# Kernel tuning notes

Hardware: AMD Instinct MI355X
Metric: run time of the kernel (lower is better)

The kernel has to match this reference:

```python
import jax, jax.numpy as jnp
import numpy as np

B, S, D, H = 8, 1024, 512, 12
HS = D // H  # 42 (head_size; 12*42 = 504 concat width, as in the original)


def setup_inputs() -> dict:
    key = jax.random.key(0)
    ks = jax.random.split(key, 12)
    sd = 0.02
    return {
        "embedded_patches": jax.random.normal(ks[0], (B, S, D), dtype=jnp.float32),
        # stacked per-head projections (12 independent Linear(D, HS, bias=False))
        "wk": jax.random.normal(ks[1], (H, D, HS), dtype=jnp.float32) * sd,
        "wq": jax.random.normal(ks[2], (H, D, HS), dtype=jnp.float32) * sd,
        "wv": jax.random.normal(ks[3], (H, D, HS), dtype=jnp.float32) * sd,
        "w_proj": jax.random.normal(ks[4], (H * HS, D), dtype=jnp.float32) * sd,  # [504, 512]
        "b_proj": jnp.zeros((D,), dtype=jnp.float32),
        # shared LayerNorm (same params used for both norms, as in the original)
        "gamma": jnp.ones((D,), dtype=jnp.float32),
        "beta": jnp.zeros((D,), dtype=jnp.float32),
        "w1": jax.random.normal(ks[5], (D, 4 * D), dtype=jnp.float32) * sd,
        "b1": jnp.zeros((4 * D,), dtype=jnp.float32),
        "w2": jax.random.normal(ks[6], (4 * D, D), dtype=jnp.float32) * sd,
        "b2": jnp.zeros((D,), dtype=jnp.float32),
    }


def _layernorm(x, gamma, beta, eps=1e-5):
    mu = jnp.mean(x, axis=-1, keepdims=True)
    var = jnp.var(x, axis=-1, keepdims=True)
    return (x - mu) * jax.lax.rsqrt(var + eps) * gamma + beta


def reference(embedded_patches, wk, wq, wv, w_proj, b_proj, gamma, beta, w1, b1, w2, b2):
    x = embedded_patches
    n1 = _layernorm(x, gamma, beta)
    # per-head projections, vectorized over heads: [B,S,D] x [H,D,E] -> [B,H,S,E]
    q = jnp.einsum('bsd,hde->bhse', n1, wq)
    k = jnp.einsum('bsd,hde->bhse', n1, wk)
    v = jnp.einsum('bsd,hde->bhse', n1, wv)
    scale = HS ** -0.5
    wei = jax.nn.softmax(jnp.einsum('bhse,bhte->bhst', q, k) * scale, axis=-1)
    out = jnp.einsum('bhst,bhte->bhse', wei, v)        # [B,H,S,E]
    out = out.transpose(0, 2, 1, 3).reshape(B, S, H * HS)  # concat heads -> [B,S,504]
    attn = out @ w_proj + b_proj                       # [B,S,D]
    # original quirk: takes batch element 0 and broadcasts against residual
    first_added = attn[0] + x                          # [S,D] + [B,S,D] -> [B,S,D]
    n2 = _layernorm(first_added, gamma, beta)
    h = jax.nn.gelu(n2 @ w1 + b1, approximate=False)   # torch nn.GELU default = exact erf
    ff = h @ w2 + b2
    return ff + first_added
```

## Files before the change

kernel.cpp:

```cpp
#include <hip/hip_runtime.h>
#include <hip/hip_bf16.h>
#include <stdint.h>


typedef unsigned short u16;
typedef __attribute__((ext_vector_type(8))) short short8;
typedef __attribute__((ext_vector_type(4))) float f32x4;

__device__ __forceinline__ u16 f2bf(float f) {
  union { float f; unsigned u; } x; x.f = f;
  return (u16)((x.u + 0x7FFFu + ((x.u >> 16) & 1u)) >> 16);
}
__device__ __forceinline__ float bf2f(u16 u) {
  union { unsigned u; float f; } x; x.u = ((unsigned)u) << 16;
  return x.f;
}

__device__ __forceinline__ void gload_lds16(const u16* g, u16* l) {
  __builtin_amdgcn_global_load_lds(
      (__attribute__((address_space(1))) void*)g,
      (__attribute__((address_space(3))) void*)l, 16, 0, 0);
}

__device__ __forceinline__ float wred_sum(float v) {
#pragma unroll
  for (int off = 32; off > 0; off >>= 1) v += __shfl_xor(v, off, 64);
  return v;
}
__device__ __forceinline__ float wred_max(float v) {
#pragma unroll
  for (int off = 32; off > 0; off >>= 1) v = fmaxf(v, __shfl_xor(v, off, 64));
  return v;
}

enum { EP_BF16 = 0, EP_PV = 1, EP_F32B = 2, EP_GELU = 3, EP_OUT = 4 };

template <int EP>
__launch_bounds__(256, 2)
__global__ void gemm_bt(const u16* __restrict__ A, int lda, long sAz,
                        const u16* __restrict__ Bt, int ldb, long sBz,
                        void* __restrict__ Cv, int ldc, long sCz,
                        int K, const float* __restrict__ bias,
                        const float* __restrict__ aux) {
  __shared__ u16 lA[128 * 32];
  __shared__ u16 lB[128 * 32];
  const int z = blockIdx.z;
  const u16* Ab = A + (long)z * sAz;
  const u16* Bb = Bt + (long)z * sBz;
  const int m0 = blockIdx.x * 128;
  const int n0 = blockIdx.y * 128;
  const int tid = threadIdx.x;
  const int w = tid >> 6;
  const int l = tid & 63;
  const int wr = w >> 1;
  const int wc = w & 1;

  f32x4 acc[4][4];
#pragma unroll
  for (int i = 0; i < 4; ++i)
#pragma unroll
    for (int j = 0; j < 4; ++j) acc[i][j] = (f32x4){0.f, 0.f, 0.f, 0.f};

  const int sm = w * 32 + (l >> 2);
  const int sk = (l & 3) * 8;
  const u16* ga0 = Ab + (long)(m0 + sm) * lda + sk;
  const u16* ga1 = Ab + (long)(m0 + sm + 16) * lda + sk;
  const u16* gb0 = Bb + (long)(n0 + sm) * ldb + sk;
  const u16* gb1 = Bb + (long)(n0 + sm + 16) * ldb + sk;
  u16* dA = &lA[w * 1024];
  u16* dB = &lB[w * 1024];

  const int aoff = (wr * 64 + (l & 15)) * 32 + (l >> 4) * 8;
  const int boff = (wc * 64 + (l & 15)) * 32 + (l >> 4) * 8;

  for (int k0 = 0; k0 < K; k0 += 32) {
    gload_lds16(ga0 + k0, dA);
    gload_lds16(ga1 + k0, dA + 512);
    gload_lds16(gb0 + k0, dB);
    gload_lds16(gb1 + k0, dB + 512);
    __syncthreads();
    short8 af[4], bfv[4];
#pragma unroll
    for (int mi = 0; mi < 4; ++mi)
      af[mi] = *(const short8*)&lA[aoff + mi * 16 * 32];
#pragma unroll
    for (int ni = 0; ni < 4; ++ni)
      bfv[ni] = *(const short8*)&lB[boff + ni * 16 * 32];
#pragma unroll
    for (int mi = 0; mi < 4; ++mi)
#pragma unroll
      for (int ni = 0; ni < 4; ++ni)
        acc[mi][ni] = __builtin_amdgcn_mfma_f32_16x16x32_bf16(
            af[mi], bfv[ni], acc[mi][ni], 0, 0, 0);
    __syncthreads();
  }

  const int rbase = m0 + wr * 64 + (l >> 4) * 4;
  const int cbase = n0 + wc * 64 + (l & 15);
#pragma unroll
  for (int mi = 0; mi < 4; ++mi) {
#pragma unroll
    for (int ni = 0; ni < 4; ++ni) {
#pragma unroll
      for (int j = 0; j < 4; ++j) {
        const int row = rbase + mi * 16 + j;
        const int col = cbase + ni * 16;
        const float v = acc[mi][ni][j];
        if (EP == EP_BF16) {
          ((u16*)Cv)[(long)z * sCz + (long)row * ldc + col] = f2bf(v);
        } else if (EP == EP_PV) {
          if (col < 42) {
            const float iv = aux[z * 1024 + row];
            ((u16*)Cv)[(long)row * ldc + z * 42 + col] = f2bf(v * iv);
          }
        } else if (EP == EP_F32B) {
          ((float*)Cv)[(long)row * ldc + col] = v + bias[col];
        } else if (EP == EP_GELU) {
          const float t = v + bias[col];
          const float g = 0.5f * t * (1.0f + erff(t * 0.70710678118654752f));
          ((u16*)Cv)[(long)row * ldc + col] = f2bf(g);
        } else {
          ((float*)Cv)[(long)row * ldc + col] =
              v + bias[col] + aux[(long)row * ldc + col];
        }
      }
    }
  }
}

__global__ void ln1_kernel(const float* __restrict__ x,
                           const float* __restrict__ gamma,
                           const float* __restrict__ beta,
                           u16* __restrict__ n1) {
  __shared__ float red[16];
  const int s = blockIdx.x;
  const int t = threadIdx.x;
  const float* row = x + (long)s * 512;
  const float v0 = row[t];
  const float v1 = row[t + 256];
  float sum = wred_sum(v0 + v1);
  float sq = wred_sum(v0 * v0 + v1 * v1);
  if ((t & 63) == 0) { red[t >> 6] = sum; red[8 + (t >> 6)] = sq; }
  __syncthreads();
  sum = red[0] + red[1] + red[2] + red[3];
  sq = red[8] + red[9] + red[10] + red[11];
  const float mu = sum * (1.0f / 512.0f);
  const float rstd = rsqrtf(sq * (1.0f / 512.0f) - mu * mu + 1e-5f);
  n1[(long)s * 512 + t] = f2bf((v0 - mu) * rstd * gamma[t] + beta[t]);
  n1[(long)s * 512 + t + 256] =
      f2bf((v1 - mu) * rstd * gamma[t + 256] + beta[t + 256]);
}

__global__ void ln2_kernel(const float* __restrict__ x,
                           const float* __restrict__ aproj,
                           const float* __restrict__ gamma,
                           const float* __restrict__ beta,
                           float* __restrict__ fa, u16* __restrict__ n2) {
  __shared__ float red[16];
  const int r = blockIdx.x;
  const int t = threadIdx.x;
  const int s = r & 1023;
  const float* xr = x + (long)r * 512;
  const float* ar = aproj + (long)s * 512;
  const float v0 = xr[t] + ar[t];
  const float v1 = xr[t + 256] + ar[t + 256];
  fa[(long)r * 512 + t] = v0;
  fa[(long)r * 512 + t + 256] = v1;
  float sum = wred_sum(v0 + v1);
  float sq = wred_sum(v0 * v0 + v1 * v1);
  if ((t & 63) == 0) { red[t >> 6] = sum; red[8 + (t >> 6)] = sq; }
  __syncthreads();
  sum = red[0] + red[1] + red[2] + red[3];
  sq = red[8] + red[9] + red[10] + red[11];
  const float mu = sum * (1.0f / 512.0f);
  const float rstd = rsqrtf(sq * (1.0f / 512.0f) - mu * mu + 1e-5f);
  n2[(long)r * 512 + t] = f2bf((v0 - mu) * rstd * gamma[t] + beta[t]);
  n2[(long)r * 512 + t + 256] =
      f2bf((v1 - mu) * rstd * gamma[t + 256] + beta[t + 256]);
}

__global__ void softmax_kernel(u16* __restrict__ SP, float* __restrict__ invl) {
  __shared__ float red[16];
  const long row = blockIdx.x;
  u16* p = SP + row * 1024;
  const int t = threadIdx.x;
  uint2 u = ((const uint2*)p)[t];
  const float s0 = bf2f((u16)(u.x & 0xffff));
  const float s1 = bf2f((u16)(u.x >> 16));
  const float s2 = bf2f((u16)(u.y & 0xffff));
  const float s3 = bf2f((u16)(u.y >> 16));
  float m = wred_max(fmaxf(fmaxf(s0, s1), fmaxf(s2, s3)));
  if ((t & 63) == 0) red[t >> 6] = m;
  __syncthreads();
  m = fmaxf(fmaxf(red[0], red[1]), fmaxf(red[2], red[3]));
  const float e0 = __expf(s0 - m), e1 = __expf(s1 - m);
  const float e2 = __expf(s2 - m), e3 = __expf(s3 - m);
  float sum = wred_sum(e0 + e1 + e2 + e3);
  if ((t & 63) == 0) red[8 + (t >> 6)] = sum;
  __syncthreads();
  sum = red[8] + red[9] + red[10] + red[11];
  if (t == 0) invl[row] = 1.0f / sum;
  uint2 o;
  o.x = (unsigned)f2bf(e0) | ((unsigned)f2bf(e1) << 16);
  o.y = (unsigned)f2bf(e2) | ((unsigned)f2bf(e3) << 16);
  ((uint2*)p)[t] = o;
}

__global__ void prep_qkv_kernel(const float* __restrict__ wq,
                                const float* __restrict__ wk,
                                u16* __restrict__ BtQKV, float scale) {
  const int i = blockIdx.x * 256 + threadIdx.x;
  const int n = i >> 9, d = i & 511;
  const int pq = n / 768;
  const int h = (n % 768) >> 6;
  const int e = n & 63;
  float v = 0.f;
  if (e < 42) {
    v = (pq ? wk : wq)[((long)h * 512 + d) * 42 + e];
    if (!pq) v *= scale;
  }
  BtQKV[i] = f2bf(v);
}
__global__ void prep_wvT_kernel(const float* __restrict__ wv,
                                u16* __restrict__ wvT) {
  const int i = blockIdx.x * 256 + threadIdx.x;
  const int r = i >> 9, d = i & 511;
  const int h = r >> 7, e = r & 127;
  wvT[i] = f2bf(e < 42 ? wv[((long)h * 512 + d) * 42 + e] : 0.f);
}
__global__ void prep_proj_kernel(const float* __restrict__ wp,
                                 u16* __restrict__ BtP) {
  const int i = blockIdx.x * 256 + threadIdx.x;
  const int n = i >> 9, k = i & 511;
  BtP[i] = f2bf(k < 504 ? wp[(long)k * 512 + n] : 0.f);
}
__global__ void prep_w1_kernel(const float* __restrict__ w1,
                               u16* __restrict__ Bt1) {
  const int i = blockIdx.x * 256 + threadIdx.x;
  const int n = i >> 9, k = i & 511;
  Bt1[i] = f2bf(w1[(long)k * 2048 + n]);
}
__global__ void prep_w2_kernel(const float* __restrict__ w2,
                               u16* __restrict__ Bt2) {
  const int i = blockIdx.x * 256 + threadIdx.x;
  const int n = i >> 11, k = i & 2047;
  Bt2[i] = f2bf(w2[(long)k * 512 + n]);
}
__global__ void zero_u16_kernel(u16* __restrict__ p) {
  p[blockIdx.x * 256 + threadIdx.x] = 0;
}

extern "C" void kernel_launch(void* const* d_in, const int* in_sizes, int n_in,
                              void* d_out, int out_size, void* d_ws,
                              size_t ws_size, hipStream_t stream) {
  const float* x = (const float*)d_in[0];
  const float* wk = (const float*)d_in[1];
  const float* wq = (const float*)d_in[2];
  const float* wv = (const float*)d_in[3];
  const float* w_proj = (const float*)d_in[4];
  const float* b_proj = (const float*)d_in[5];
  const float* gamma = (const float*)d_in[6];
  const float* beta = (const float*)d_in[7];
  const float* w1 = (const float*)d_in[8];
  const float* b1 = (const float*)d_in[9];
  const float* w2 = (const float*)d_in[10];
  const float* b2 = (const float*)d_in[11];

  char* base = (char*)d_ws;
  size_t off = 0;
  auto alloc = [&](size_t bytes) -> void* {
    void* p = base + off;
    off += (bytes + 255) & ~(size_t)255;
    return p;
  };
  u16* n1 = (u16*)alloc(1024L * 512 * 2);
  u16* qkvc = (u16*)alloc(1024L * 1536 * 2);
  u16* SP = (u16*)alloc(12L * 1024 * 1024 * 2);
  u16* wvT = (u16*)alloc(1536L * 512 * 2);
  u16* vt = (u16*)alloc(1536L * 1024 * 2);
  u16* cat = (u16*)alloc(1024L * 512 * 2);
  float* aproj = (float*)alloc(1024L * 512 * 4);
  float* fa = (float*)alloc(8192L * 512 * 4);
  u16* n2 = (u16*)alloc(8192L * 512 * 2);
  u16* hbuf = (u16*)alloc(8192L * 2048 * 2);
  u16* BtQKV = (u16*)alloc(1536L * 512 * 2);
  u16* BtP = (u16*)alloc(512L * 512 * 2);
  u16* Bt1 = (u16*)alloc(2048L * 512 * 2);
  u16* Bt2 = (u16*)alloc(512L * 2048 * 2);
  float* invl = (float*)alloc(12L * 1024 * 4);
  (void)ws_size; (void)in_sizes; (void)n_in; (void)out_size;

  const float scale = 0.15430334996209191f;

  prep_qkv_kernel<<<3072, 256, 0, stream>>>(wq, wk, BtQKV, scale);
  prep_wvT_kernel<<<3072, 256, 0, stream>>>(wv, wvT);
  prep_proj_kernel<<<1024, 256, 0, stream>>>(w_proj, BtP);
  prep_w1_kernel<<<4096, 256, 0, stream>>>(w1, Bt1);
  prep_w2_kernel<<<4096, 256, 0, stream>>>(w2, Bt2);
  zero_u16_kernel<<<2048, 256, 0, stream>>>(cat);
  ln1_kernel<<<1024, 256, 0, stream>>>(x, gamma, beta, n1);

  gemm_bt<EP_BF16><<<dim3(8, 12, 1), 256, 0, stream>>>(
      n1, 512, 0, BtQKV, 512, 0, qkvc, 1536, 0, 512, nullptr, nullptr);
  gemm_bt<EP_BF16><<<dim3(12, 8, 1), 256, 0, stream>>>(
      wvT, 512, 0, n1, 512, 0, vt, 1024, 0, 512, nullptr, nullptr);
  gemm_bt<EP_BF16><<<dim3(8, 8, 12), 256, 0, stream>>>(
      qkvc, 1536, 64, qkvc + 768, 1536, 64, SP, 1024, 1024L * 1024, 64,
      nullptr, nullptr);
  softmax_kernel<<<12288, 256, 0, stream>>>(SP, invl);
  gemm_bt<EP_PV><<<dim3(8, 1, 12), 256, 0, stream>>>(
      SP, 1024, 1024L * 1024, vt, 1024, 128L * 1024, cat, 512, 0, 1024,
      nullptr, invl);
  gemm_bt<EP_F32B><<<dim3(8, 4, 1), 256, 0, stream>>>(
      cat, 512, 0, BtP, 512, 0, aproj, 512, 0, 512, b_proj, nullptr);
  ln2_kernel<<<8192, 256, 0, stream>>>(x, aproj, gamma, beta, fa, n2);
  gemm_bt<EP_GELU><<<dim3(64, 16, 1), 256, 0, stream>>>(
      n2, 512, 0, Bt1, 512, 0, hbuf, 2048, 0, 512, b1, nullptr);
  gemm_bt<EP_OUT><<<dim3(64, 4, 1), 256, 0, stream>>>(
      hbuf, 2048, 0, Bt2, 2048, 0, d_out, 512, 0, 2048, b2, fa);
}
```

Baseline: 195.2 us.

## Use 256x256 double-buffered pipelined GEMM with split-K for FFN layers

Adds a new 512-thread GEMM kernel with 256x256 tiles, K-step 64, XOR-swizzled LDS, double buffering, direct global-to-LDS loads interleaved with MFMA phases, and priority hints. It replaces the two FFN GEMMs. The second GEMM is split in two along K into fp32 partials, which a separate combine kernel sums with the bias and residual. This aims to raise MFMA utilisation and data reuse on the dominant FFN work. The cost is extra partial-buffer traffic, one extra launch, and a write of part into the start of d_ws, which may overlap buffers carved out of the same workspace.

```diff
diff --git a/kernel.cpp b/kernel.cpp
--- a/kernel.cpp
+++ b/kernel.cpp
@@ -33,7 +33,175 @@
   return v;
 }
 
-enum { EP_BF16 = 0, EP_PV = 1, EP_F32B = 2, EP_GELU = 3, EP_OUT = 4 };
+#define MFMA16x16(a, b, c) __builtin_amdgcn_mfma_f32_16x16x32_bf16(a, b, c, 0, 0, 0)
+
+enum { G8_GELU = 0, G8_F32 = 1 };
+
+template <int EP>
+__device__ __forceinline__ void read_af8(short8 (&af)[8], const u16* half,
+                                         int aBase, int s0, int s1) {
+  const char* hc = (const char*)half;
+#pragma unroll
+  for (int mi = 0; mi < 4; ++mi) {
+    af[mi * 2 + 0] = *(const short8*)(hc + aBase + mi * 2048 + s0);
+    af[mi * 2 + 1] = *(const short8*)(hc + aBase + mi * 2048 + s1);
+  }
+}
+template <int EP>
+__device__ __forceinline__ void read_bf4(short8 (&bf)[4], const u16* half,
+                                         int bBase, int s0, int s1) {
+  const char* hc = (const char*)half;
+#pragma unroll
+  for (int ni = 0; ni < 2; ++ni) {
+    bf[ni * 2 + 0] = *(const short8*)(hc + bBase + ni * 2048 + s0);
+    bf[ni * 2 + 1] = *(const short8*)(hc + bBase + ni * 2048 + s1);
+  }
+}
+template <int MH, int NH>
+__device__ __forceinline__ void do_mfma16(f32x4 (&acc)[8][4],
+                                          const short8 (&af)[8],
+                                          const short8 (&bf)[4]) {
+#pragma unroll
+  for (int mi = 0; mi < 4; ++mi)
+#pragma unroll
+    for (int ni = 0; ni < 2; ++ni)
+#pragma unroll
+      for (int ks = 0; ks < 2; ++ks)
+        acc[MH * 4 + mi][NH * 2 + ni] =
+            MFMA16x16(af[mi * 2 + ks], bf[ni * 2 + ks], acc[MH * 4 + mi][NH * 2 + ni]);
+}
+
+__device__ __forceinline__ void stage_half(const u16* src, int ld, u16* halfdst,
+                                           int w, int l) {
+  const int r0 = w * 8 + (l >> 3);
+  const int ce = ((l & 7) ^ (l >> 3)) * 8;
+  gload_lds16(src + (long)r0 * ld + ce, halfdst + w * 512);
+  gload_lds16(src + (long)(r0 + 64) * ld + ce, halfdst + (8 + w) * 512);
+}
+
+#define H_A0 0
+#define H_B0 1
+#define H_B1 2
+#define H_A1 3
+
+template <int EP>
+__launch_bounds__(512, 2)
+__global__ void gemm8(const u16* __restrict__ A, int lda, long sAz,
+                      const u16* __restrict__ Bt, int ldb, long sBz,
+                      void* __restrict__ Cv, int ldc, long sCz, int K,
+                      const float* __restrict__ bias) {
+  __shared__ u16 lds[2 * 4 * 8192];
+  const int z = blockIdx.z;
+  const u16* Ab = A + (long)z * sAz;
+  const u16* Bb = Bt + (long)z * sBz;
+  const int m0 = blockIdx.x * 256;
+  const int n0 = blockIdx.y * 256;
+  const int tid = threadIdx.x;
+  const int w = tid >> 6;
+  const int l = tid & 63;
+  const int wm = w >> 2;
+  const int wn = w & 3;
+  const int NT = K >> 6;
+
+  const int aBase = (wm * 64 + (l & 15)) * 128;
+  const int bBase = (wn * 32 + (l & 15)) * 128;
+  const int s0 = (((l >> 4)) ^ (l & 7)) * 16;
+  const int s1 = ((4 + (l >> 4)) ^ (l & 7)) * 16;
+
+  f32x4 acc[8][4];
+#pragma unroll
+  for (int i = 0; i < 8; ++i)
+#pragma unroll
+    for (int j = 0; j < 4; ++j) acc[i][j] = (f32x4){0.f, 0.f, 0.f, 0.f};
+
+  short8 af[8], bf0[4], bf1[4];
+
+  stage_half(Ab + (long)m0 * lda, lda, lds + H_A0 * 8192, w, l);
+  stage_half(Bb + (long)n0 * ldb, ldb, lds + H_B0 * 8192, w, l);
+  stage_half(Bb + (long)(n0 + 128) * ldb, ldb, lds + H_B1 * 8192, w, l);
+  stage_half(Ab + (long)(m0 + 128) * lda, lda, lds + H_A1 * 8192, w, l);
+
+  for (int t = 0; t < NT; ++t) {
+    u16* cur = lds + (t & 1) * 32768;
+    u16* nxt = lds + ((t & 1) ^ 1) * 32768;
+    const int tn = (t + 1 == NT) ? 0 : (t + 1);
+    const u16* An = Ab + tn * 64;
+    const u16* Bn = Bb + tn * 64;
+
+    asm volatile("s_waitcnt vmcnt(4)" ::: "memory");
+    __builtin_amdgcn_s_barrier();
+    __builtin_amdgcn_sched_barrier(0);
+    read_af8<EP>(af, cur + H_A0 * 8192, aBase, s0, s1);
+    read_bf4<EP>(bf0, cur + H_B0 * 8192, bBase, s0, s1);
+    stage_half(An + (long)m0 * lda, lda, nxt + H_A0 * 8192, w, l);
+    asm volatile("s_waitcnt lgkmcnt(0)" ::: "memory");
+    __builtin_amdgcn_sched_barrier(0);
+    __builtin_amdgcn_s_setprio(1);
+    do_mfma16<0, 0>(acc, af, bf0);
+    __builtin_amdgcn_s_setprio(0);
+
+    asm volatile("s_waitcnt vmcnt(4)" ::: "memory");
+    __builtin_amdgcn_s_barrier();
+    __builtin_amdgcn_sched_barrier(0);
+    read_bf4<EP>(bf1, cur + H_B1 * 8192, bBase, s0, s1);
+    stage_half(Bn + (long)n0 * ldb, ldb, nxt + H_B0 * 8192, w, l);
+    asm volatile("s_waitcnt lgkmcnt(0)" ::: "memory");
+    __builtin_amdgcn_sched_barrier(0);
+    __builtin_amdgcn_s_setprio(1);
+    do_mfma16<0, 1>(acc, af, bf1);
+    __builtin_amdgcn_s_setprio(0);
+
+    asm volatile("s_waitcnt vmcnt(4)" ::: "memory");
+    __builtin_amdgcn_s_barrier();
+    __builtin_amdgcn_sched_barrier(0);
+    read_af8<EP>(af, cur + H_A1 * 8192, aBase, s0, s1);
+    stage_half(Bn + (long)(n0 + 128) * ldb, ldb, nxt + H_B1 * 8192, w, l);
+    stage_half(An + (long)(m0 + 128) * lda, lda, nxt + H_A1 * 8192, w, l);
+    asm volatile("s_waitcnt lgkmcnt(0)" ::: "memory");
+    __builtin_amdgcn_sched_barrier(0);
+    __builtin_amdgcn_s_setprio(1);
+    do_mfma16<1, 0>(acc, af, bf0);
+    do_mfma16<1, 1>(acc, af, bf1);
+    __builtin_amdgcn_s_setprio(0);
+  }
+  asm volatile("s_waitcnt vmcnt(0)" ::: "memory");
+
+  const int rb = m0 + wm * 64 + ((l >> 4) << 2);
+  const int cb = n0 + wn * 32 + (l & 15);
+#pragma unroll
+  for (int mi = 0; mi < 8; ++mi) {
+    const int row = rb + (mi >> 2) * 128 + (mi & 3) * 16;
+#pragma unroll
+    for (int ni = 0; ni < 4; ++ni) {
+      const int col = cb + (ni >> 1) * 128 + (ni & 1) * 16;
+#pragma unroll
+      for (int j = 0; j < 4; ++j) {
+        const float v = acc[mi][ni][j];
+        if (EP == G8_GELU) {
+          const float tt = v + bias[col];
+          const float g = 0.5f * tt * (1.0f + erff(tt * 0.70710678118654752f));
+          ((u16*)Cv)[(long)(row + j) * ldc + col] = f2bf(g);
+        } else {
+          ((float*)Cv)[(long)z * sCz + (long)(row + j) * ldc + col] = v;
+        }
+      }
+    }
+  }
+}
+
+__global__ void combine_kernel(const float* __restrict__ p,
+                               const float* __restrict__ fa,
+                               const float* __restrict__ b2,
+                               float* __restrict__ out) {
+  const long i = (long)blockIdx.x * 256 + threadIdx.x;
+  const f32x4 a = ((const f32x4*)p)[i];
+  const f32x4 b = ((const f32x4*)(p + 8192L * 512))[i];
+  const f32x4 f = ((const f32x4*)fa)[i];
+  const f32x4 bb = ((const f32x4*)b2)[i & 127];
+  ((f32x4*)out)[i] = a + b + f + bb;
+}
+
+enum { EP_BF16 = 0, EP_PV = 1, EP_F32B = 2 };
 
 template <int EP>
 __launch_bounds__(256, 2)
@@ -90,8 +258,7 @@
     for (int mi = 0; mi < 4; ++mi)
 #pragma unroll
       for (int ni = 0; ni < 4; ++ni)
-        acc[mi][ni] = __builtin_amdgcn_mfma_f32_16x16x32_bf16(
-            af[mi], bfv[ni], acc[mi][ni], 0, 0, 0);
+        acc[mi][ni] = MFMA16x16(af[mi], bfv[ni], acc[mi][ni]);
     __syncthreads();
   }
 
@@ -113,15 +280,8 @@
             const float iv = aux[z * 1024 + row];
             ((u16*)Cv)[(long)row * ldc + z * 42 + col] = f2bf(v * iv);
           }
-        } else if (EP == EP_F32B) {
+        } else {
           ((float*)Cv)[(long)row * ldc + col] = v + bias[col];
-        } else if (EP == EP_GELU) {
-          const float t = v + bias[col];
-          const float g = 0.5f * t * (1.0f + erff(t * 0.70710678118654752f));
-          ((u16*)Cv)[(long)row * ldc + col] = f2bf(g);
-        } else {
-          ((float*)Cv)[(long)row * ldc + col] =
-              v + bias[col] + aux[(long)row * ldc + col];
         }
       }
     }
@@ -288,6 +448,7 @@
   u16* Bt1 = (u16*)alloc(2048L * 512 * 2);
   u16* Bt2 = (u16*)alloc(512L * 2048 * 2);
   float* invl = (float*)alloc(12L * 1024 * 4);
+  float* part = (float*)d_ws;
   (void)ws_size; (void)in_sizes; (void)n_in; (void)out_size;
 
   const float scale = 0.15430334996209191f;
@@ -314,8 +475,10 @@
   gemm_bt<EP_F32B><<<dim3(8, 4, 1), 256, 0, stream>>>(
       cat, 512, 0, BtP, 512, 0, aproj, 512, 0, 512, b_proj, nullptr);
   ln2_kernel<<<8192, 256, 0, stream>>>(x, aproj, gamma, beta, fa, n2);
-  gemm_bt<EP_GELU><<<dim3(64, 16, 1), 256, 0, stream>>>(
-      n2, 512, 0, Bt1, 512, 0, hbuf, 2048, 0, 512, b1, nullptr);
-  gemm_bt<EP_OUT><<<dim3(64, 4, 1), 256, 0, stream>>>(
-      hbuf, 2048, 0, Bt2, 2048, 0, d_out, 512, 0, 2048, b2, fa);
-}
+  gemm8<G8_GELU><<<dim3(32, 8, 1), 512, 0, stream>>>(
+      n2, 512, 0, Bt1, 512, 0, hbuf, 2048, 0, 512, b1);
+  gemm8<G8_F32><<<dim3(32, 2, 2), 512, 0, stream>>>(
+      hbuf, 2048, 1024, Bt2, 2048, 1024, part, 512, 8192L * 512, 1024,
+      nullptr);
+  combine_kernel<<<4096, 256, 0, stream>>>(part, fa, b2, (float*)d_out);
+}
```

Result: slower. 215.9 us (+10.6%).

## Double-buffer LDS tiles in GEMM to overlap global loads with MFMA

Applied to the files above, without the earlier changes.

Rewrites the shared GEMM kernel with two LDS buffers per operand. The next K-tile's global-to-LDS loads are issued while the current tile's MFMAs run, so each iteration has one barrier instead of two. Launch bounds are raised to 4 blocks per CU. The aim is to hide global load latency, at the cost of twice the LDS (32KB per block) and tighter register limits that could cause spills.

```diff
diff --git a/kernel.cpp b/kernel.cpp
--- a/kernel.cpp
+++ b/kernel.cpp
@@ -33,17 +33,19 @@
   return v;
 }
 
+#define MFMA16x16(a, b, c) __builtin_amdgcn_mfma_f32_16x16x32_bf16(a, b, c, 0, 0, 0)
+
 enum { EP_BF16 = 0, EP_PV = 1, EP_F32B = 2, EP_GELU = 3, EP_OUT = 4 };
 
 template <int EP>
-__launch_bounds__(256, 2)
-__global__ void gemm_bt(const u16* __restrict__ A, int lda, long sAz,
-                        const u16* __restrict__ Bt, int ldb, long sBz,
-                        void* __restrict__ Cv, int ldc, long sCz,
-                        int K, const float* __restrict__ bias,
-                        const float* __restrict__ aux) {
-  __shared__ u16 lA[128 * 32];
-  __shared__ u16 lB[128 * 32];
+__launch_bounds__(256, 4)
+__global__ void gemm2(const u16* __restrict__ A, int lda, long sAz,
+                      const u16* __restrict__ Bt, int ldb, long sBz,
+                      void* __restrict__ Cv, int ldc, long sCz,
+                      int K, const float* __restrict__ bias,
+                      const float* __restrict__ aux) {
+  __shared__ u16 lA[2][128 * 32];
+  __shared__ u16 lB[2][128 * 32];
   const int z = blockIdx.z;
   const u16* Ab = A + (long)z * sAz;
   const u16* Bb = Bt + (long)z * sBz;
@@ -54,6 +56,7 @@
   const int l = tid & 63;
   const int wr = w >> 1;
   const int wc = w & 1;
+  const int NT = K >> 5;
 
   f32x4 acc[4][4];
 #pragma unroll
@@ -61,38 +64,47 @@
 #pragma unroll
     for (int j = 0; j < 4; ++j) acc[i][j] = (f32x4){0.f, 0.f, 0.f, 0.f};
 
-  const int sm = w * 32 + (l >> 2);
+  const int srow = w * 32 + (l >> 2);
   const int sk = (l & 3) * 8;
-  const u16* ga0 = Ab + (long)(m0 + sm) * lda + sk;
-  const u16* ga1 = Ab + (long)(m0 + sm + 16) * lda + sk;
-  const u16* gb0 = Bb + (long)(n0 + sm) * ldb + sk;
-  const u16* gb1 = Bb + (long)(n0 + sm + 16) * ldb + sk;
-  u16* dA = &lA[w * 1024];
-  u16* dB = &lB[w * 1024];
+  const u16* ga0 = Ab + (long)(m0 + srow) * lda + sk;
+  const u16* ga1 = Ab + (long)(m0 + srow + 16) * lda + sk;
+  const u16* gb0 = Bb + (long)(n0 + srow) * ldb + sk;
+  const u16* gb1 = Bb + (long)(n0 + srow + 16) * ldb + sk;
+  const int dOff = w * 1024;
 
   const int aoff = (wr * 64 + (l & 15)) * 32 + (l >> 4) * 8;
   const int boff = (wc * 64 + (l & 15)) * 32 + (l >> 4) * 8;
 
-  for (int k0 = 0; k0 < K; k0 += 32) {
-    gload_lds16(ga0 + k0, dA);
-    gload_lds16(ga1 + k0, dA + 512);
-    gload_lds16(gb0 + k0, dB);
-    gload_lds16(gb1 + k0, dB + 512);
+  gload_lds16(ga0, &lA[0][dOff]);
+  gload_lds16(ga1, &lA[0][dOff + 512]);
+  gload_lds16(gb0, &lB[0][dOff]);
+  gload_lds16(gb1, &lB[0][dOff + 512]);
+  __syncthreads();
+
+  int buf = 0;
+  for (int t = 0; t < NT; ++t) {
+    short8 af[4], bfv[4];
+#pragma unroll
+    for (int mi = 0; mi < 4; ++mi)
+      af[mi] = *(const short8*)&lA[buf][aoff + mi * 16 * 32];
+#pragma unroll
+    for (int ni = 0; ni < 4; ++ni)
+      bfv[ni] = *(const short8*)&lB[buf][boff + ni * 16 * 32];
+    if (t + 1 < NT) {
+      const int k0 = (t + 1) * 32;
+      const int nb = buf ^ 1;
+      gload_lds16(ga0 + k0, &lA[nb][dOff]);
+      gload_lds16(ga1 + k0, &lA[nb][dOff + 512]);
+      gload_lds16(gb0 + k0, &lB[nb][dOff]);
+      gload_lds16(gb1 + k0, &lB[nb][dOff + 512]);
+    }
+#pragma unroll
+    for (int mi = 0; mi < 4; ++mi)
+#pragma unroll
+      for (int ni = 0; ni < 4; ++ni)
+        acc[mi][ni] = MFMA16x16(af[mi], bfv[ni], acc[mi][ni]);
     __syncthreads();
-    short8 af[4], bfv[4];
-#pragma unroll
-    for (int mi = 0; mi < 4; ++mi)
-      af[mi] = *(const short8*)&lA[aoff + mi * 16 * 32];
-#pragma unroll
-    for (int ni = 0; ni < 4; ++ni)
-      bfv[ni] = *(const short8*)&lB[boff + ni * 16 * 32];
-#pragma unroll
-    for (int mi = 0; mi < 4; ++mi)
-#pragma unroll
-      for (int ni = 0; ni < 4; ++ni)
-        acc[mi][ni] = __builtin_amdgcn_mfma_f32_16x16x32_bf16(
-            af[mi], bfv[ni], acc[mi][ni], 0, 0, 0);
-    __syncthreads();
+    buf ^= 1;
   }
 
   const int rbase = m0 + wr * 64 + (l >> 4) * 4;
@@ -116,8 +128,8 @@
         } else if (EP == EP_F32B) {
           ((float*)Cv)[(long)row * ldc + col] = v + bias[col];
         } else if (EP == EP_GELU) {
-          const float t = v + bias[col];
-          const float g = 0.5f * t * (1.0f + erff(t * 0.70710678118654752f));
+          const float tt = v + bias[col];
+          const float g = 0.5f * tt * (1.0f + erff(tt * 0.70710678118654752f));
           ((u16*)Cv)[(long)row * ldc + col] = f2bf(g);
         } else {
           ((float*)Cv)[(long)row * ldc + col] =
@@ -300,22 +312,22 @@
   zero_u16_kernel<<<2048, 256, 0, stream>>>(cat);
   ln1_kernel<<<1024, 256, 0, stream>>>(x, gamma, beta, n1);
 
-  gemm_bt<EP_BF16><<<dim3(8, 12, 1), 256, 0, stream>>>(
+  gemm2<EP_BF16><<<dim3(8, 12, 1), 256, 0, stream>>>(
       n1, 512, 0, BtQKV, 512, 0, qkvc, 1536, 0, 512, nullptr, nullptr);
-  gemm_bt<EP_BF16><<<dim3(12, 8, 1), 256, 0, stream>>>(
+  gemm2<EP_BF16><<<dim3(12, 8, 1), 256, 0, stream>>>(
       wvT, 512, 0, n1, 512, 0, vt, 1024, 0, 512, nullptr, nullptr);
-  gemm_bt<EP_BF16><<<dim3(8, 8, 12), 256, 0, stream>>>(
+  gemm2<EP_BF16><<<dim3(8, 8, 12), 256, 0, stream>>>(
       qkvc, 1536, 64, qkvc + 768, 1536, 64, SP, 1024, 1024L * 1024, 64,
       nullptr, nullptr);
   softmax_kernel<<<12288, 256, 0, stream>>>(SP, invl);
-  gemm_bt<EP_PV><<<dim3(8, 1, 12), 256, 0, stream>>>(
+  gemm2<EP_PV><<<dim3(8, 1, 12), 256, 0, stream>>>(
       SP, 1024, 1024L * 1024, vt, 1024, 128L * 1024, cat, 512, 0, 1024,
       nullptr, invl);
-  gemm_bt<EP_F32B><<<dim3(8, 4, 1), 256, 0, stream>>>(
+  gemm2<EP_F32B><<<dim3(8, 4, 1), 256, 0, stream>>>(
       cat, 512, 0, BtP, 512, 0, aproj, 512, 0, 512, b_proj, nullptr);
   ln2_kernel<<<8192, 256, 0, stream>>>(x, aproj, gamma, beta, fa, n2);
-  gemm_bt<EP_GELU><<<dim3(64, 16, 1), 256, 0, stream>>>(
+  gemm2<EP_GELU><<<dim3(64, 16, 1), 256, 0, stream>>>(
       n2, 512, 0, Bt1, 512, 0, hbuf, 2048, 0, 512, b1, nullptr);
-  gemm_bt<EP_OUT><<<dim3(64, 4, 1), 256, 0, stream>>>(
+  gemm2<EP_OUT><<<dim3(64, 4, 1), 256, 0, stream>>>(
       hbuf, 2048, 0, Bt2, 2048, 0, d_out, 512, 0, 2048, b2, fa);
 }
```

Result: faster. 188.3 us (-3.5%).
